# Performance work log

Measured on AMD Instinct MI355X. Metric: run time of the kernel, lower is better.

The kernel has to match this reference:

```python
import jax, jax.numpy as jnp
import numpy as np

B, N, D, C, S = 128, 100000, 256, 2000, 751  # batch, memory size, feat dim, num classes, source classes
TEMP = 0.05
EPS = 1e-06


def _l2norm(x):
    return x / jnp.linalg.norm(x, axis=-1, keepdims=True)


def setup_inputs() -> dict:
    key = jax.random.key(0)
    k1, k2, k3, k4, k5 = jax.random.split(key, 5)
    inputs = _l2norm(jax.random.normal(k1, (B, D), dtype=jnp.float32))
    inputs2 = _l2norm(jax.random.normal(k2, (B, D), dtype=jnp.float32))
    features = _l2norm(jax.random.normal(k3, (N, D), dtype=jnp.float32))
    labels = jax.random.randint(k4, (N,), 0, C)
    labels = labels.at[:C].set(jnp.arange(C))  # ensure labels.max()+1 == C
    indexes = jax.random.randint(k5, (B,), 0, N)
    return {"inputs": inputs, "inputs2": inputs2, "features": features,
            "labels": labels, "indexes": indexes, "source_classes": S}


def reference(inputs, inputs2, features, labels, indexes, source_classes):
    # memory-bank logits, [B, N]
    logits = (inputs @ features.T) / TEMP
    logits2 = (inputs2 @ features.T) / TEMP
    targets = labels[indexes]  # [B]

    # per-class counts and segment-mean of logits over the bank, [C, B]
    nums = jax.ops.segment_sum(jnp.ones((N,), jnp.float32), labels, num_segments=C)  # [C]
    denom = jnp.where(nums > 0, nums, 1.0)[:, None]  # [C, 1]
    sim = jax.ops.segment_sum(logits.T, labels, num_segments=C) / denom   # [C, B]
    sim2 = jax.ops.segment_sum(logits2.T, labels, num_segments=C) / denom  # [C, B]

    # MSE between class-probability maps over the first source_classes classes
    p1 = sim[:source_classes].T   # [B, S]
    p2 = sim2[:source_classes].T  # [B, S]
    diff = jax.nn.softmax(p1, axis=1) - jax.nn.softmax(p2, axis=1)
    loss_mse = jnp.sum(diff * diff) / source_classes

    # hard-positive/negative mining: per-class max of logits (0 for empty classes)
    seg_max = jax.ops.segment_max(logits.T, labels, num_segments=C)  # [C, B], -inf where empty
    present = (nums > 0)  # [C]
    sim_hard = jnp.where(present[:, None], seg_max, 0.0).T  # [B, C]
    # for the target class, use the hardest (min) positive instead
    seg_min = jax.ops.segment_min(logits.T, labels, num_segments=C)  # [C, B]
    b_idx = jnp.arange(B)
    sim_hard = sim_hard.at[b_idx, targets].set(seg_min[targets, b_idx])

    # masked softmax over present classes + NLL
    mask = present.astype(jnp.float32)[None, :]  # [1, C]
    exps = jnp.exp(sim_hard) * mask
    masked_sim = exps / (jnp.sum(exps, axis=1, keepdims=True) + EPS)
    loss_con = -jnp.mean(jnp.log(masked_sim[b_idx, targets] + EPS))

    return (loss_con, loss_mse)
```

## Files before the change

### kernel.cpp

```cpp
#include <hip/hip_runtime.h>
#include <hip/hip_bf16.h>

#define BB 128
#define NN 100000
#define DD 256
#define CC 2000
#define SS 751
#define INVTEMP 20.0f
#define EPSV 1e-6f

#define HIST_BLOCKS 391
#define PREP_BLOCKS 32
#define NTILES_MAX 3563

typedef __attribute__((ext_vector_type(8))) short bf16x8;
typedef __attribute__((ext_vector_type(8))) unsigned short u16x8;
typedef __attribute__((ext_vector_type(4))) float f32x4;

__device__ __forceinline__ unsigned short f2bf(float x) {
    unsigned int u = __float_as_uint(x);
    u += 0x7fffu + ((u >> 16) & 1u);
    return (unsigned short)(u >> 16);
}

__device__ __forceinline__ u16x8 cvt8u(float4 a, float4 b) {
    union { unsigned u[4]; u16x8 v; } cv;
    asm("v_cvt_pk_bf16_f32 %0, %1, %2" : "=v"(cv.u[0]) : "v"(a.x), "v"(a.y));
    asm("v_cvt_pk_bf16_f32 %0, %1, %2" : "=v"(cv.u[1]) : "v"(a.z), "v"(a.w));
    asm("v_cvt_pk_bf16_f32 %0, %1, %2" : "=v"(cv.u[2]) : "v"(b.x), "v"(b.y));
    asm("v_cvt_pk_bf16_f32 %0, %1, %2" : "=v"(cv.u[3]) : "v"(b.z), "v"(b.w));
    return cv.v;
}

__global__ __launch_bounds__(256) void hist_prep_kernel(
    const int* __restrict__ labels, int* __restrict__ counts,
    const float* __restrict__ in1, const float* __restrict__ in2,
    unsigned short* __restrict__ inb)
{
    int bid = blockIdx.x;
    if (bid < HIST_BLOCKS) {
        int n = bid * 256 + threadIdx.x;
        if (n < NN) atomicAdd(&counts[labels[n]], 1);
    } else {
        int ch = (bid - HIST_BLOCKS) * 256 + threadIdx.x;
        if (ch >= 8192) return;
        int l  = ch & 63;
        int kc = (ch >> 6) & 7;
        int nr = ch >> 9;
        int row = nr * 16 + (l & 15);
        const float* src = (row < BB) ? (in1 + (size_t)row * DD)
                                      : (in2 + (size_t)(row - BB) * DD);
        int k0 = kc * 32 + ((l >> 4) << 3);
        u16x8 o;
        #pragma unroll
        for (int j = 0; j < 8; ++j) o[j] = f2bf(src[k0 + j]);
        *(u16x8*)(inb + (size_t)ch * 8) = o;
    }
}

__global__ __launch_bounds__(256) void scan_kernel(const int* __restrict__ counts,
                                                   int* __restrict__ tile_start,
                                                   int* __restrict__ cursor,
                                                   int* __restrict__ tile_meta,
                                                   int* __restrict__ ntiles_total,
                                                   float* __restrict__ out) {
    const int PT = 8;
    int tid = threadIdx.x;
    if (tid == 0) { out[0] = 0.f; out[1] = 0.f; }
    int tcnt[PT];
    int tot = 0;
    #pragma unroll
    for (int i = 0; i < PT; ++i) {
        int c = tid * PT + i;
        tcnt[i] = (c < CC) ? ((counts[c] + 63) >> 6) : 0;
        tot += tcnt[i];
    }
    __shared__ int sh[256];
    sh[tid] = tot;
    __syncthreads();
    for (int ofs = 1; ofs < 256; ofs <<= 1) {
        int v = (tid >= ofs) ? sh[tid - ofs] : 0;
        __syncthreads();
        sh[tid] += v;
        __syncthreads();
    }
    if (tid == 255) *ntiles_total = sh[255];
    int run = sh[tid] - tot;
    #pragma unroll
    for (int i = 0; i < PT; ++i) {
        int c = tid * PT + i;
        if (c < CC) {
            tile_start[c] = run;
            cursor[c] = run << 6;
            for (int j = 0; j < tcnt[i]; ++j)
                tile_meta[run + j] = (c << 5) | j;
        }
        run += tcnt[i];
    }
}

__global__ void scatter_idx(const int* __restrict__ labels, int* __restrict__ cursor,
                            int* __restrict__ sorted_idx) {
    int n = blockIdx.x * 256 + threadIdx.x;
    if (n < NN) {
        int c = labels[n];
        int p = atomicAdd(&cursor[c], 1);
        sorted_idx[p] = n;
    }
}

__global__ __launch_bounds__(512, 4) void mm_kernel(
    const float* __restrict__ features, const unsigned short* __restrict__ inb,
    const int* __restrict__ sorted_idx, const int* __restrict__ tile_meta,
    const int* __restrict__ counts, const int* __restrict__ ntiles_total,
    float* __restrict__ part_max, float* __restrict__ part_min,
    float* __restrict__ part_sA, float* __restrict__ part_sB)
{
    const int t = blockIdx.x;
    if (t >= *ntiles_total) return;
    const int tid = threadIdx.x;
    const int w   = tid >> 6;
    const int l   = tid & 63;
    const int meta = tile_meta[t];
    const int base_local = (meta & 31) << 6;
    const int cnt  = counts[meta >> 5];
    const int vrows = cnt - base_local;

    __shared__ __align__(16) char ldsA[32768];

    bf16x8 bfr[16];
    #pragma unroll
    for (int kc = 0; kc < 8; ++kc)
        #pragma unroll
        for (int nb = 0; nb < 2; ++nb)
            bfr[kc * 2 + nb] = *(const bf16x8*)(inb + (((size_t)((2 * w + nb) * 8 + kc) * 64 + l) << 3));

    {
        const int m0 = tid >> 3;
        const int g  = tid & 7;
        int idx = t * 64 + ((m0 < vrows) ? m0 : 0);
        int n   = sorted_idx[idx];
        const float* src = features + (size_t)n * DD + g * 8;
        float4 R[8];
        #pragma unroll
        for (int s = 0; s < 4; ++s) {
            R[2 * s]     = *(const float4*)(src + s * 64);
            R[2 * s + 1] = *(const float4*)(src + s * 64 + 4);
        }
        const int ma = m0 >> 4;
        #pragma unroll
        for (int s = 0; s < 4; ++s) {
            u16x8 o = cvt8u(R[2 * s], R[2 * s + 1]);
            int crow = s * 8 + g;
            int kc   = crow >> 2;
            int ks   = crow & 3;
            int cch  = (ks << 4) | ((m0 & 15) ^ kc);
            *(u16x8*)(&ldsA[0] + (((ma * 8 + kc) << 10) | (cch << 4))) = o;
        }
    }

    #pragma unroll
    for (int i = 0; i < 16; ++i)
        asm volatile("" : "+v"(bfr[i]));

    __syncthreads();

    f32x4 acc[4][2];
    #pragma unroll
    for (int ma = 0; ma < 4; ++ma)
        #pragma unroll
        for (int nb = 0; nb < 2; ++nb)
            acc[ma][nb] = (f32x4){0.f, 0.f, 0.f, 0.f};

    #pragma unroll
    for (int kc = 0; kc < 8; ++kc) {
        int lx = (l ^ kc) << 4;
        #pragma unroll
        for (int ma = 0; ma < 4; ++ma) {
            bf16x8 a = *(const bf16x8*)(&ldsA[0] + ((ma * 8 + kc) << 10) + lx);
            acc[ma][0] = __builtin_amdgcn_mfma_f32_16x16x32_bf16(a, bfr[kc * 2 + 0], acc[ma][0], 0, 0, 0);
            acc[ma][1] = __builtin_amdgcn_mfma_f32_16x16x32_bf16(a, bfr[kc * 2 + 1], acc[ma][1], 0, 0, 0);
        }
    }

    const int h4 = (l >> 4) << 2;
    const bool do_mm = (w < 4);
    float sm[2] = {0.f, 0.f};
    float mx[2] = {-3.4e38f, -3.4e38f};
    float mn[2] = { 3.4e38f,  3.4e38f};
    #pragma unroll
    for (int ma = 0; ma < 4; ++ma) {
        #pragma unroll
        for (int reg = 0; reg < 4; ++reg) {
            bool valid = (16 * ma + h4 + reg) < vrows;
            if (valid) {
                #pragma unroll
                for (int nb = 0; nb < 2; ++nb) {
                    float v = acc[ma][nb][reg];
                    sm[nb] += v;
                    if (do_mm) {
                        mx[nb] = fmaxf(mx[nb], v);
                        mn[nb] = fminf(mn[nb], v);
                    }
                }
            }
        }
    }
    #pragma unroll
    for (int nb = 0; nb < 2; ++nb) {
        sm[nb] += __shfl_xor(sm[nb], 16);
        sm[nb] += __shfl_xor(sm[nb], 32);
        if (do_mm) {
            mx[nb] = fmaxf(mx[nb], __shfl_xor(mx[nb], 16));
            mx[nb] = fmaxf(mx[nb], __shfl_xor(mx[nb], 32));
            mn[nb] = fminf(mn[nb], __shfl_xor(mn[nb], 16));
            mn[nb] = fminf(mn[nb], __shfl_xor(mn[nb], 32));
        }
    }
    if (l < 16) {
        #pragma unroll
        for (int nb = 0; nb < 2; ++nb) {
            int col = 32 * (w & 3) + 16 * nb + l;
            size_t p = (size_t)t * 128 + col;
            if (do_mm) { part_max[p] = mx[nb]; part_min[p] = mn[nb]; part_sA[p] = sm[nb]; }
            else       { part_sB[p] = sm[nb]; }
        }
    }
}


__device__ __forceinline__ float blk_reduce_sum(float v) {
    __shared__ float sh[4];
    int lane = threadIdx.x & 63, w = threadIdx.x >> 6;
    #pragma unroll
    for (int o = 32; o; o >>= 1) v += __shfl_down(v, o, 64);
    __syncthreads();
    if (lane == 0) sh[w] = v;
    __syncthreads();
    return sh[0] + sh[1] + sh[2] + sh[3];
}

__device__ __forceinline__ float blk_reduce_max(float v) {
    __shared__ float sh[4];
    int lane = threadIdx.x & 63, w = threadIdx.x >> 6;
    #pragma unroll
    for (int o = 32; o; o >>= 1) v = fmaxf(v, __shfl_down(v, o, 64));
    __syncthreads();
    if (lane == 0) sh[w] = v;
    __syncthreads();
    return fmaxf(fmaxf(sh[0], sh[1]), fmaxf(sh[2], sh[3]));
}

__global__ __launch_bounds__(256) void finalize_kernel(
    const float* __restrict__ part_max, const float* __restrict__ part_min,
    const float* __restrict__ part_sA, const float* __restrict__ part_sB,
    const int* __restrict__ tile_start, const int* __restrict__ counts,
    const int* __restrict__ labels, const int* __restrict__ indexes,
    float* __restrict__ out)
{
    const int b   = blockIdx.x;
    const int tid = threadIdx.x;
    const int tgt = labels[indexes[b]];

    __shared__ float a1[SS], a2[SS];
    __shared__ float sh_etgt;

    float local = 0.f;
    for (int c = tid; c < CC; c += 256) {
        int cnt = counts[c];
        if (cnt > 0) {
            int t0 = tile_start[c];
            int nt = (cnt + 63) >> 6;
            bool src = (c < SS);
            float mx = -3.4e38f, sA = 0.f, sB = 0.f;
            for (int j = 0; j < nt; ++j) {
                size_t p = (size_t)(t0 + j) * 128 + b;
                mx = fmaxf(mx, part_max[p]);
                if (src) { sA += part_sA[p]; sB += part_sB[p]; }
            }
            float v = mx;
            if (c == tgt) {
                float mn = 3.4e38f;
                for (int j = 0; j < nt; ++j)
                    mn = fminf(mn, part_min[(size_t)(t0 + j) * 128 + b]);
                v = mn;
            }
            float e = expf(v * INVTEMP);
            local += e;
            if (c == tgt) sh_etgt = e;
            if (src) {
                float icnt = INVTEMP / (float)cnt;
                a1[c] = sA * icnt;
                a2[c] = sB * icnt;
            }
        } else if (c < SS) {
            a1[c] = 0.f;
            a2[c] = 0.f;
        }
    }
    float sum_e = blk_reduce_sum(local);
    float etgt = sh_etgt;
    float loss_con_b = -logf(etgt / (sum_e + EPSV) + EPSV);

    float m1 = -3.4e38f, m2 = -3.4e38f;
    for (int c = tid; c < SS; c += 256) { m1 = fmaxf(m1, a1[c]); m2 = fmaxf(m2, a2[c]); }
    m1 = blk_reduce_max(m1);
    m2 = blk_reduce_max(m2);
    float s1 = 0.f, s2 = 0.f;
    for (int c = tid; c < SS; c += 256) { s1 += expf(a1[c] - m1); s2 += expf(a2[c] - m2); }
    s1 = blk_reduce_sum(s1);
    s2 = blk_reduce_sum(s2);
    float inv1 = 1.f / s1, inv2 = 1.f / s2;
    float dsum = 0.f;
    for (int c = tid; c < SS; c += 256) {
        float d = expf(a1[c] - m1) * inv1 - expf(a2[c] - m2) * inv2;
        dsum += d * d;
    }
    dsum = blk_reduce_sum(dsum);
    if (tid == 0) {
        atomicAdd(&out[0], loss_con_b * (1.0f / (float)BB));
        atomicAdd(&out[1], dsum * (1.0f / (float)SS));
    }
}


extern "C" void kernel_launch(void* const* d_in, const int* in_sizes, int n_in,
                              void* d_out, int out_size, void* d_ws, size_t ws_size,
                              hipStream_t stream) {
    const float* inputs   = (const float*)d_in[0];
    const float* inputs2  = (const float*)d_in[1];
    const float* features = (const float*)d_in[2];
    const int*   labels   = (const int*)d_in[3];
    const int*   indexes  = (const int*)d_in[4];

    float* out = (float*)d_out;

    int* wsi = (int*)d_ws;
    int* counts     = wsi;
    int* tile_start = wsi + 2048;
    int* cursor     = wsi + 4096;
    int* ntiles     = wsi + 6144;
    unsigned short* inb = (unsigned short*)(wsi + 6160);
    int* tile_meta  = wsi + 38928;
    int* sorted_idx = wsi + 42496;
    float* part_max = (float*)(wsi + 270592);
    float* part_min = part_max + (size_t)NTILES_MAX * 128;
    float* part_sA  = part_min + (size_t)NTILES_MAX * 128;
    float* part_sB  = part_sA  + (size_t)NTILES_MAX * 128;

    hipMemsetAsync(counts, 0, 2048 * sizeof(int), stream);

    hist_prep_kernel<<<HIST_BLOCKS + PREP_BLOCKS, 256, 0, stream>>>(
        labels, counts, inputs, inputs2, inb);
    scan_kernel<<<1, 256, 0, stream>>>(counts, tile_start, cursor, tile_meta, ntiles, out);
    scatter_idx<<<HIST_BLOCKS, 256, 0, stream>>>(labels, cursor, sorted_idx);
    mm_kernel<<<NTILES_MAX, 512, 0, stream>>>(features, inb, sorted_idx, tile_meta,
                                              counts, ntiles,
                                              part_max, part_min, part_sA, part_sB);
    finalize_kernel<<<BB, 256, 0, stream>>>(part_max, part_min, part_sA, part_sB,
                                            tile_start, counts, labels, indexes, out);
}
```

Before: 91.12 us.

## Merge histogram, scan and scatter into one cooperative kernel with grid syncs

Replaces the three preprocessing launches (histogram plus input bf16 prep, single-block scan, index scatter) with one cooperative kernel that uses grid.sync between phases. The aim is to remove two kernel launch gaps from a short pipeline. In exchange it adds the cost of cooperative launch and grid-wide barriers, runs the serial scan on one block while the others sit idle, and uses fewer threads (256 blocks with grid-stride loops).

```diff
diff --git a/kernel.cpp b/kernel.cpp
--- a/kernel.cpp
+++ b/kernel.cpp
@@ -1,5 +1,8 @@
 #include <hip/hip_runtime.h>
 #include <hip/hip_bf16.h>
+#include <hip/hip_cooperative_groups.h>
+
+namespace cg = cooperative_groups;
 
 #define BB 128
 #define NN 100000
@@ -9,9 +12,9 @@
 #define INVTEMP 20.0f
 #define EPSV 1e-6f
 
-#define HIST_BLOCKS 391
-#define PREP_BLOCKS 32
 #define NTILES_MAX 3563
+#define COOP_BLOCKS 256
+#define COOP_THREADS 65536
 
 typedef __attribute__((ext_vector_type(8))) short bf16x8;
 typedef __attribute__((ext_vector_type(8))) unsigned short u16x8;
@@ -32,77 +35,75 @@
     return cv.v;
 }
 
-__global__ __launch_bounds__(256) void hist_prep_kernel(
+__global__ __launch_bounds__(256) void prep_coop(
     const int* __restrict__ labels, int* __restrict__ counts,
     const float* __restrict__ in1, const float* __restrict__ in2,
-    unsigned short* __restrict__ inb)
+    unsigned short* __restrict__ inb,
+    int* __restrict__ tile_start, int* __restrict__ cursor,
+    int* __restrict__ tile_meta, int* __restrict__ ntiles_total,
+    float* __restrict__ out, int* __restrict__ sorted_idx)
 {
-    int bid = blockIdx.x;
-    if (bid < HIST_BLOCKS) {
-        int n = bid * 256 + threadIdx.x;
-        if (n < NN) atomicAdd(&counts[labels[n]], 1);
-    } else {
-        int ch = (bid - HIST_BLOCKS) * 256 + threadIdx.x;
-        if (ch >= 8192) return;
-        int l  = ch & 63;
-        int kc = (ch >> 6) & 7;
-        int nr = ch >> 9;
-        int row = nr * 16 + (l & 15);
-        const float* src = (row < BB) ? (in1 + (size_t)row * DD)
-                                      : (in2 + (size_t)(row - BB) * DD);
-        int k0 = kc * 32 + ((l >> 4) << 3);
-        u16x8 o;
-        #pragma unroll
-        for (int j = 0; j < 8; ++j) o[j] = f2bf(src[k0 + j]);
-        *(u16x8*)(inb + (size_t)ch * 8) = o;
-    }
-}
-
-__global__ __launch_bounds__(256) void scan_kernel(const int* __restrict__ counts,
-                                                   int* __restrict__ tile_start,
-                                                   int* __restrict__ cursor,
-                                                   int* __restrict__ tile_meta,
-                                                   int* __restrict__ ntiles_total,
-                                                   float* __restrict__ out) {
-    const int PT = 8;
-    int tid = threadIdx.x;
-    if (tid == 0) { out[0] = 0.f; out[1] = 0.f; }
-    int tcnt[PT];
-    int tot = 0;
-    #pragma unroll
-    for (int i = 0; i < PT; ++i) {
-        int c = tid * PT + i;
-        tcnt[i] = (c < CC) ? ((counts[c] + 63) >> 6) : 0;
-        tot += tcnt[i];
-    }
-    __shared__ int sh[256];
-    sh[tid] = tot;
-    __syncthreads();
-    for (int ofs = 1; ofs < 256; ofs <<= 1) {
-        int v = (tid >= ofs) ? sh[tid - ofs] : 0;
+    cg::grid_group grid = cg::this_grid();
+    const int gtid = blockIdx.x * 256 + threadIdx.x;
+
+    for (int i = gtid; i < 8192 + NN; i += COOP_THREADS) {
+        if (i < 8192) {
+            int l  = i & 63;
+            int kc = (i >> 6) & 7;
+            int nr = i >> 9;
+            int row = nr * 16 + (l & 15);
+            const float* src = (row < BB) ? (in1 + (size_t)row * DD)
+                                          : (in2 + (size_t)(row - BB) * DD);
+            int k0 = kc * 32 + ((l >> 4) << 3);
+            u16x8 o;
+            #pragma unroll
+            for (int j = 0; j < 8; ++j) o[j] = f2bf(src[k0 + j]);
+            *(u16x8*)(inb + (size_t)i * 8) = o;
+        } else {
+            int n = i - 8192;
+            atomicAdd(&counts[labels[n]], 1);
+        }
+    }
+    grid.sync();
+
+    if (blockIdx.x == 0) {
+        const int PT = 8;
+        int tid = threadIdx.x;
+        if (tid == 0) { out[0] = 0.f; out[1] = 0.f; }
+        int tcnt[PT];
+        int tot = 0;
+        #pragma unroll
+        for (int i = 0; i < PT; ++i) {
+            int c = tid * PT + i;
+            tcnt[i] = (c < CC) ? ((counts[c] + 63) >> 6) : 0;
+            tot += tcnt[i];
+        }
+        __shared__ int sh[256];
+        sh[tid] = tot;
         __syncthreads();
-        sh[tid] += v;
-        __syncthreads();
-    }
-    if (tid == 255) *ntiles_total = sh[255];
-    int run = sh[tid] - tot;
-    #pragma unroll
-    for (int i = 0; i < PT; ++i) {
-        int c = tid * PT + i;
-        if (c < CC) {
-            tile_start[c] = run;
-            cursor[c] = run << 6;
-            for (int j = 0; j < tcnt[i]; ++j)
-                tile_meta[run + j] = (c << 5) | j;
-        }
-        run += tcnt[i];
-    }
-}
-
-__global__ void scatter_idx(const int* __restrict__ labels, int* __restrict__ cursor,
-                            int* __restrict__ sorted_idx) {
-    int n = blockIdx.x * 256 + threadIdx.x;
-    if (n < NN) {
+        for (int ofs = 1; ofs < 256; ofs <<= 1) {
+            int v = (tid >= ofs) ? sh[tid - ofs] : 0;
+            __syncthreads();
+            sh[tid] += v;
+            __syncthreads();
+        }
+        if (tid == 255) *ntiles_total = sh[255];
+        int run = sh[tid] - tot;
+        #pragma unroll
+        for (int i = 0; i < PT; ++i) {
+            int c = tid * PT + i;
+            if (c < CC) {
+                tile_start[c] = run;
+                cursor[c] = run << 6;
+                for (int j = 0; j < tcnt[i]; ++j)
+                    tile_meta[run + j] = (c << 5) | j;
+            }
+            run += tcnt[i];
+        }
+    }
+    grid.sync();
+
+    for (int n = gtid; n < NN; n += COOP_THREADS) {
         int c = labels[n];
         int p = atomicAdd(&cursor[c], 1);
         sorted_idx[p] = n;
@@ -350,10 +351,16 @@
 
     hipMemsetAsync(counts, 0, 2048 * sizeof(int), stream);
 
-    hist_prep_kernel<<<HIST_BLOCKS + PREP_BLOCKS, 256, 0, stream>>>(
-        labels, counts, inputs, inputs2, inb);
-    scan_kernel<<<1, 256, 0, stream>>>(counts, tile_start, cursor, tile_meta, ntiles, out);
-    scatter_idx<<<HIST_BLOCKS, 256, 0, stream>>>(labels, cursor, sorted_idx);
+    {
+        void* args[] = {
+            (void*)&labels, (void*)&counts, (void*)&inputs, (void*)&inputs2,
+            (void*)&inb, (void*)&tile_start, (void*)&cursor, (void*)&tile_meta,
+            (void*)&ntiles, (void*)&out, (void*)&sorted_idx
+        };
+        hipLaunchCooperativeKernel((const void*)prep_coop, dim3(COOP_BLOCKS), dim3(256),
+                                   args, 0, stream);
+    }
+
     mm_kernel<<<NTILES_MAX, 512, 0, stream>>>(features, inb, sorted_idx, tile_meta,
                                               counts, ntiles,
                                               part_max, part_min, part_sA, part_sB);
```

Result: slower. 148.5 us (+62.9%).
